# Kernel tuning notes

Hardware: AMD Instinct MI355X
Metric: run time of the kernel (lower is better)

The kernel has to match this reference:

```python
import jax, jax.numpy as jnp
import numpy as np

D = 256      # dim
H = 8        # num_heads
HD = D // H  # head dim
P = 256      # patch_size
B = 4        # num clouds
L = 32768    # points per cloud (divisible by P)
N = B * L
MLP = int(D * 2.0)
PEH = max(32, D // 4)
EPS = 1e-5


def setup_inputs() -> dict:
    key = jax.random.key(0)
    ks = jax.random.split(key, 20)
    s = 0.02
    w = lambda k, shp: jax.random.normal(k, shp, jnp.float32) * s
    inp = {
        "feats": jax.random.normal(ks[0], (N, D), jnp.float32),
        "coord": jax.random.uniform(ks[1], (N, 3), jnp.float32),
        "lengths": jnp.full((B,), L, jnp.int32),
        # CoordPositionalEncoding: Linear(3,PEH) -> ReLU -> Linear(PEH,D)
        "pe_w1": w(ks[2], (3, PEH)), "pe_b1": jnp.zeros((PEH,), jnp.float32),
        "pe_w2": w(ks[3], (PEH, D)), "pe_b2": jnp.zeros((D,), jnp.float32),
        "pre_g": jnp.ones((D,), jnp.float32), "pre_b": jnp.zeros((D,), jnp.float32),
        # block: norm1 + MHA + norm2 + MLP
        "n1_g": jnp.ones((D,), jnp.float32), "n1_b": jnp.zeros((D,), jnp.float32),
        "wqkv": w(ks[4], (D, 3 * D)), "bqkv": jnp.zeros((3 * D,), jnp.float32),
        "wo": w(ks[5], (D, D)), "bo": jnp.zeros((D,), jnp.float32),
        "n2_g": jnp.ones((D,), jnp.float32), "n2_b": jnp.zeros((D,), jnp.float32),
        "m_w1": w(ks[6], (D, MLP)), "m_b1": jnp.zeros((MLP,), jnp.float32),
        "m_w2": w(ks[7], (MLP, D)), "m_b2": jnp.zeros((D,), jnp.float32),
        # global_gate: Linear(2D,D)->ReLU->Linear(D,D)->Sigmoid
        "gg_w1": w(ks[8], (2 * D, D)), "gg_b1": jnp.zeros((D,), jnp.float32),
        "gg_w2": w(ks[9], (D, D)), "gg_b2": jnp.zeros((D,), jnp.float32),
        # fuse: Linear(2D,D)->ReLU->Linear(D,D)
        "f_w1": w(ks[10], (2 * D, D)), "f_b1": jnp.zeros((D,), jnp.float32),
        "f_w2": w(ks[11], (D, D)), "f_b2": jnp.zeros((D,), jnp.float32),
    }
    return inp


def _ln(x, g, b):
    m = x.mean(-1, keepdims=True)
    v = jnp.mean((x - m) ** 2, -1, keepdims=True)
    return (x - m) * jax.lax.rsqrt(v + EPS) * g + b


def _sgca(feats, coord, lengths,
          pe_w1, pe_b1, pe_w2, pe_b2, pre_g, pre_b,
          n1_g, n1_b, wqkv, bqkv, wo, bo, n2_g, n2_b,
          m_w1, m_b1, m_w2, m_b2,
          gg_w1, gg_b1, gg_w2, gg_b2, f_w1, f_b1, f_w2, f_b2):
    Bn = lengths.shape[0]
    Ln = feats.shape[0] // Bn  # equal-length clouds

    def cloud(f, c):  # f: [L, D], c: [L, 3]
        # positional encoding (per-cloud centered / max-abs scaled coords)
        cc = c - c.mean(0, keepdims=True)
        scale = jnp.clip(jnp.abs(cc).max(0, keepdims=True), 1e-6)
        pe = jax.nn.relu((cc / scale) @ pe_w1 + pe_b1) @ pe_w2 + pe_b2
        x = _ln(f + pe, pre_g, pre_b)
        # serialization order from min-max normalized coords
        cn = c - c.min(0, keepdims=True)
        cn = cn / jnp.clip(cn.max(0, keepdims=True), 1e-6)
        key = cn[:, 0] + 2.17 * cn[:, 1] + 3.31 * cn[:, 2]
        order = jnp.argsort(key)
        xs = x[order].reshape(-1, P, D)  # [NP, P, D] block-diagonal windows
        # attention block (pre-norm MHA + residual)
        h = _ln(xs, n1_g, n1_b)
        qkv = h @ wqkv + bqkv
        q = qkv[..., :D].reshape(-1, P, H, HD)
        k = qkv[..., D:2 * D].reshape(-1, P, H, HD)
        v = qkv[..., 2 * D:].reshape(-1, P, H, HD)
        scores = jnp.einsum('nphd,nqhd->nhpq', q, k) / np.sqrt(HD).astype(np.float32)
        a = jax.nn.softmax(scores, axis=-1)
        o = jnp.einsum('nhpq,nqhd->nphd', a, v).reshape(-1, P, D)
        xs = xs + (o @ wo + bo)
        # MLP + residual
        xs = xs + (jax.nn.gelu(_ln(xs, n2_g, n2_b) @ m_w1 + m_b1, approximate=False) @ m_w2 + m_b2)
        # undo serialization
        xo = xs.reshape(-1, D)[jnp.argsort(order)]
        # global token gate/fuse
        gt = jnp.broadcast_to(xo.mean(0, keepdims=True), xo.shape)
        gate = jax.nn.sigmoid(jax.nn.relu(jnp.concatenate([f, gt], -1) @ gg_w1 + gg_b1) @ gg_w2 + gg_b2)
        fused = jax.nn.relu(jnp.concatenate([xo, gt], -1) @ f_w1 + f_b1) @ f_w2 + f_b2
        return f + gate * fused

    out = jax.vmap(cloud)(feats.reshape(Bn, Ln, D), coord.reshape(Bn, Ln, 3))
    return out.reshape(-1, D)


def reference(feats, coord, lengths,
              pe_w1, pe_b1, pe_w2, pe_b2, pre_g, pre_b,
              n1_g, n1_b, wqkv, bqkv, wo, bo, n2_g, n2_b,
              m_w1, m_b1, m_w2, m_b2,
              gg_w1, gg_b1, gg_w2, gg_b2, f_w1, f_b1, f_w2, f_b2):
    return _sgca(feats, coord, lengths,
                 pe_w1, pe_b1, pe_w2, pe_b2, pre_g, pre_b,
                 n1_g, n1_b, wqkv, bqkv, wo, bo, n2_g, n2_b,
                 m_w1, m_b1, m_w2, m_b2,
                 gg_w1, gg_b1, gg_w2, gg_b2, f_w1, f_b1, f_w2, f_b2)
```

## Files before the change

kernel.cpp:

```cpp
#include <hip/hip_runtime.h>
#include <hip/hip_bf16.h>
#include <math.h>

#define D_DIM 256
#define NHEAD 8
#define HDIM 32
#define PATCH 256
#define NCLOUD 4
#define LPC 32768
#define NTOT (NCLOUD * LPC)
#define MLPD 512
#define PEHID 64
#define LN_EPS 1e-5f
#define NCHUNK 4
#define CROWS (NTOT / NCHUNK)

typedef unsigned long long u64;
typedef unsigned short u16;
typedef short bf16x8 __attribute__((ext_vector_type(8)));
typedef float f32x4 __attribute__((ext_vector_type(4)));

__device__ __forceinline__ u16 f2bf(float x) {
  unsigned u = __float_as_uint(x);
  u += 0x7fffu + ((u >> 16) & 1u);
  return (u16)(u >> 16);
}
__device__ __forceinline__ float bf2f(u16 u) {
  return __uint_as_float(((unsigned)u) << 16);
}

__device__ __forceinline__ void gload_lds16(const u16* g, u16* l) {
  __builtin_amdgcn_global_load_lds((const __attribute__((address_space(1))) void*)g,
                                   (__attribute__((address_space(3))) void*)l, 16, 0, 0);
}

__global__ __launch_bounds__(256) void stats_kernel(const float* __restrict__ coord,
                                                    float* __restrict__ stats) {
  const int c = blockIdx.x, t = threadIdx.x;
  float sm[3] = {0.f, 0.f, 0.f};
  float mn[3] = {1e30f, 1e30f, 1e30f};
  float mx[3] = {-1e30f, -1e30f, -1e30f};
  const float* cp = coord + (size_t)c * LPC * 3;
  for (int i = t; i < LPC; i += 256) {
#pragma unroll
    for (int a = 0; a < 3; a++) {
      float v = cp[(size_t)i * 3 + a];
      sm[a] += v;
      mn[a] = fminf(mn[a], v);
      mx[a] = fmaxf(mx[a], v);
    }
  }
  __shared__ float sb[256];
  float rsum[3], rmn[3], rmx[3];
#pragma unroll
  for (int a = 0; a < 3; a++) {
    sb[t] = sm[a]; __syncthreads();
    for (int s = 128; s > 0; s >>= 1) { if (t < s) sb[t] += sb[t + s]; __syncthreads(); }
    rsum[a] = sb[0]; __syncthreads();
    sb[t] = mn[a]; __syncthreads();
    for (int s = 128; s > 0; s >>= 1) { if (t < s) sb[t] = fminf(sb[t], sb[t + s]); __syncthreads(); }
    rmn[a] = sb[0]; __syncthreads();
    sb[t] = mx[a]; __syncthreads();
    for (int s = 128; s > 0; s >>= 1) { if (t < s) sb[t] = fmaxf(sb[t], sb[t + s]); __syncthreads(); }
    rmx[a] = sb[0]; __syncthreads();
  }
  if (t == 0) {
    float* st = stats + c * 16;
#pragma unroll
    for (int a = 0; a < 3; a++) {
      float mean = rsum[a] / (float)LPC;
      st[a] = mean;
      st[3 + a] = fmaxf(fmaxf(rmx[a] - mean, mean - rmn[a]), 1e-6f);
      st[6 + a] = rmn[a];
      st[9 + a] = fmaxf(rmx[a] - rmn[a], 1e-6f);
    }
  }
}

__global__ __launch_bounds__(256) void key_kernel(const float* __restrict__ coord,
                                                  const float* __restrict__ stats,
                                                  u64* __restrict__ keys) {
#pragma clang fp contract(off)
  const int g = blockIdx.x * 256 + threadIdx.x;
  const int c = g >> 15;
  const float* st = stats + c * 16;
  float k0 = (coord[(size_t)g * 3 + 0] - st[6]) / st[9];
  float k1 = (coord[(size_t)g * 3 + 1] - st[7]) / st[10];
  float k2 = (coord[(size_t)g * 3 + 2] - st[8]) / st[11];
  float key = k0 + 2.17f * k1;
  key = key + 3.31f * k2;
  keys[g] = ((u64)__float_as_uint(key) << 32) | (unsigned)(g & (LPC - 1));
}

__global__ __launch_bounds__(256) void sort_local_kernel(u64* __restrict__ keys) {
  __shared__ u64 s[4096];
  const int base = blockIdx.x * 4096;
  const int t = threadIdx.x;
  for (int i = t; i < 4096; i += 256) s[i] = keys[base + i];
  __syncthreads();
  for (int k = 2; k <= 4096; k <<= 1) {
    for (int j = k >> 1; j > 0; j >>= 1) {
      for (int p = t; p < 2048; p += 256) {
        int i = ((p & ~(j - 1)) << 1) | (p & (j - 1));
        int l = i | j;
        bool asc = (((base + i) & (LPC - 1)) & k) == 0;
        u64 a = s[i], bb = s[l];
        if (asc ? (a > bb) : (a < bb)) { s[i] = bb; s[l] = a; }
      }
      __syncthreads();
    }
  }
  for (int i = t; i < 4096; i += 256) keys[base + i] = s[i];
}

__global__ __launch_bounds__(256) void sort_global_kernel(u64* __restrict__ keys, int k, int j) {
  int p = blockIdx.x * 256 + threadIdx.x;
  int i = ((p & ~(j - 1)) << 1) | (p & (j - 1));
  int l = i | j;
  bool asc = ((i & (LPC - 1)) & k) == 0;
  u64 a = keys[i], b = keys[l];
  if (asc ? (a > b) : (a < b)) { keys[i] = b; keys[l] = a; }
}

__global__ __launch_bounds__(256) void sort_finish_kernel(u64* __restrict__ keys, int k) {
  __shared__ u64 s[4096];
  const int base = blockIdx.x * 4096;
  const int t = threadIdx.x;
  for (int i = t; i < 4096; i += 256) s[i] = keys[base + i];
  __syncthreads();
  for (int j = 2048; j > 0; j >>= 1) {
    for (int p = t; p < 2048; p += 256) {
      int i = ((p & ~(j - 1)) << 1) | (p & (j - 1));
      int l = i | j;
      bool asc = (((base + i) & (LPC - 1)) & k) == 0;
      u64 a = s[i], bb = s[l];
      if (asc ? (a > bb) : (a < bb)) { s[i] = bb; s[l] = a; }
    }
    __syncthreads();
  }
  for (int i = t; i < 4096; i += 256) keys[base + i] = s[i];
}

__global__ __launch_bounds__(256) void rank_kernel(const u64* __restrict__ keys,
                                                   int* __restrict__ order,
                                                   int* __restrict__ rank) {
  const int g = blockIdx.x * 256 + threadIdx.x;
  const int src = (int)(unsigned)(keys[g] & 0xffffffffULL) + (g & ~(LPC - 1));
  order[g] = src;
  rank[src] = g;
}

__global__ __launch_bounds__(256) void wtrans_kernel(const float* __restrict__ src,
                                                     u16* __restrict__ dst, int R, int C) {
  __shared__ float t[32][33];
  const int bx = blockIdx.x * 32, by = blockIdx.y * 32;
  const int lc = threadIdx.x & 31, lr = threadIdx.x >> 5;
  for (int i = 0; i < 32; i += 8) t[lr + i][lc] = src[(size_t)(by + lr + i) * C + bx + lc];
  __syncthreads();
  for (int i = 0; i < 32; i += 8)
    dst[(size_t)(bx + lr + i) * R + by + lc] = f2bf(t[lc][lr + i]);
}

__global__ __launch_bounds__(256) void conv_bf16_kernel(const float* __restrict__ in,
                                                        u16* __restrict__ out) {
  size_t i = ((size_t)blockIdx.x * 256 + threadIdx.x) * 4;
  float4 v = *(const float4*)(in + i);
  ushort4 o;
  o.x = f2bf(v.x); o.y = f2bf(v.y); o.z = f2bf(v.z); o.w = f2bf(v.w);
  *(ushort4*)(out + i) = o;
}

__global__ __launch_bounds__(256) void h_kernel(const float* __restrict__ coord,
                                                const float* __restrict__ stats,
                                                const float* __restrict__ pw1,
                                                const float* __restrict__ pb1,
                                                u16* __restrict__ H) {
  const int idx = blockIdx.x * 256 + threadIdx.x;
  const int row = idx >> 6, j = idx & 63;
  const int c = row >> 15;
  const float* st = stats + c * 16;
  float s0 = (coord[(size_t)row * 3 + 0] - st[0]) / st[3];
  float s1 = (coord[(size_t)row * 3 + 1] - st[1]) / st[4];
  float s2 = (coord[(size_t)row * 3 + 2] - st[2]) / st[5];
  float h = pb1[j] + s0 * pw1[j] + s1 * pw1[64 + j] + s2 * pw1[128 + j];
  H[idx] = f2bf(fmaxf(h, 0.f));
}

__global__ __launch_bounds__(256) void add_ln_kernel(const float* __restrict__ feats,
                                                     const u16* __restrict__ pe,
                                                     const int* __restrict__ rank,
                                                     const float* __restrict__ g,
                                                     const float* __restrict__ b,
                                                     float* __restrict__ xs) {
  const int row = blockIdx.x * 4 + (threadIdx.x >> 6);
  const int lane = threadIdx.x & 63;
  float4 f = *(const float4*)(feats + (size_t)row * 256 + lane * 4);
  ushort4 p = *(const ushort4*)(pe + (size_t)row * 256 + lane * 4);
  float v0 = f.x + bf2f(p.x), v1 = f.y + bf2f(p.y);
  float v2 = f.z + bf2f(p.z), v3 = f.w + bf2f(p.w);
  float s = v0 + v1 + v2 + v3;
#pragma unroll
  for (int o = 32; o > 0; o >>= 1) s += __shfl_xor(s, o);
  float mean = s * (1.f / 256.f);
  float d0 = v0 - mean, d1 = v1 - mean, d2 = v2 - mean, d3 = v3 - mean;
  float ss = d0 * d0 + d1 * d1 + d2 * d2 + d3 * d3;
#pragma unroll
  for (int o = 32; o > 0; o >>= 1) ss += __shfl_xor(ss, o);
  float inv = 1.f / sqrtf(ss * (1.f / 256.f) + LN_EPS);
  float4 gv = *(const float4*)(g + lane * 4);
  float4 bv = *(const float4*)(b + lane * 4);
  int dst = rank[row];
  float4 o4;
  o4.x = d0 * inv * gv.x + bv.x; o4.y = d1 * inv * gv.y + bv.y;
  o4.z = d2 * inv * gv.z + bv.z; o4.w = d3 * inv * gv.w + bv.w;
  *(float4*)(xs + (size_t)dst * 256 + lane * 4) = o4;
}

__global__ __launch_bounds__(256) void ln_bf16_kernel(const float* __restrict__ in,
                                                      const float* __restrict__ g,
                                                      const float* __restrict__ b,
                                                      u16* __restrict__ out) {
  const int row = blockIdx.x * 4 + (threadIdx.x >> 6);
  const int lane = threadIdx.x & 63;
  float4 v = *(const float4*)(in + (size_t)row * 256 + lane * 4);
  float s = v.x + v.y + v.z + v.w;
#pragma unroll
  for (int o = 32; o > 0; o >>= 1) s += __shfl_xor(s, o);
  float mean = s * (1.f / 256.f);
  float d0 = v.x - mean, d1 = v.y - mean, d2 = v.z - mean, d3 = v.w - mean;
  float ss = d0 * d0 + d1 * d1 + d2 * d2 + d3 * d3;
#pragma unroll
  for (int o = 32; o > 0; o >>= 1) ss += __shfl_xor(ss, o);
  float inv = 1.f / sqrtf(ss * (1.f / 256.f) + LN_EPS);
  float4 gv = *(const float4*)(g + lane * 4);
  float4 bv = *(const float4*)(b + lane * 4);
  ushort4 o4;
  o4.x = f2bf(d0 * inv * gv.x + bv.x); o4.y = f2bf(d1 * inv * gv.y + bv.y);
  o4.z = f2bf(d2 * inv * gv.z + bv.z); o4.w = f2bf(d3 * inv * gv.w + bv.w);
  *(ushort4*)(out + (size_t)row * 256 + lane * 4) = o4;
}

__global__ __launch_bounds__(256) void scatter_bf16_kernel(const int* __restrict__ order,
                                                           const float* __restrict__ xs,
                                                           u16* __restrict__ xo) {
  const int row = blockIdx.x * 4 + (threadIdx.x >> 6);
  const int lane = threadIdx.x & 63;
  float4 v = *(const float4*)(xs + (size_t)row * 256 + lane * 4);
  const int dst = order[row];
  ushort4 o;
  o.x = f2bf(v.x); o.y = f2bf(v.y); o.z = f2bf(v.z); o.w = f2bf(v.w);
  *(ushort4*)(xo + (size_t)dst * 256 + lane * 4) = o;
}

template <int K, int ACT, int MODE, bool EXTRA>
__global__ __launch_bounds__(256, 4) void mfma_gemm(const u16* __restrict__ A,
                                                    const u16* __restrict__ Wt,
                                                    const float* __restrict__ bias,
                                                    const float* __restrict__ extra,
                                                    void* __restrict__ Cout,
                                                    const u16* __restrict__ gate,
                                                    const float* __restrict__ feats, int Ko) {
  __shared__ __align__(16) u16 Al[128 * 32];
  __shared__ __align__(16) u16 Bl[128 * 32];
  const int tid = threadIdx.x;
  const int lane = tid & 63, wave = tid >> 6;
  const int wr = wave >> 1, wc = wave & 1;
  const int l15 = lane & 15, l4 = lane >> 4;
  const size_t row0 = (size_t)blockIdx.y * 128;
  const int col0 = blockIdx.x * 128;
  const int q0 = wave * 64 + lane;
  const int q1 = q0 + 256;
  const u16* gA0 = A + (row0 + (q0 >> 2)) * K + (q0 & 3) * 8;
  const u16* gA1 = A + (row0 + (q1 >> 2)) * K + (q1 & 3) * 8;
  const u16* gB0 = Wt + (size_t)(col0 + (q0 >> 2)) * K + (q0 & 3) * 8;
  const u16* gB1 = Wt + (size_t)(col0 + (q1 >> 2)) * K + (q1 & 3) * 8;
  u16* lA0 = Al + wave * 512;
  u16* lA1 = Al + 2048 + wave * 512;
  u16* lB0 = Bl + wave * 512;
  u16* lB1 = Bl + 2048 + wave * 512;
  f32x4 acc[4][4];
#pragma unroll
  for (int i = 0; i < 4; i++)
#pragma unroll
    for (int j = 0; j < 4; j++) acc[i][j] = f32x4{0.f, 0.f, 0.f, 0.f};
#pragma unroll 1
  for (int k0 = 0; k0 < K; k0 += 32) {
    gload_lds16(gA0 + k0, lA0);
    gload_lds16(gA1 + k0, lA1);
    gload_lds16(gB0 + k0, lB0);
    gload_lds16(gB1 + k0, lB1);
    __syncthreads();
    bf16x8 af[4], bfr[4];
#pragma unroll
    for (int rb = 0; rb < 4; rb++)
      af[rb] = *(const bf16x8*)&Al[(wr * 64 + rb * 16 + l15) * 32 + l4 * 8];
#pragma unroll
    for (int cb = 0; cb < 4; cb++)
      bfr[cb] = *(const bf16x8*)&Bl[(wc * 64 + cb * 16 + l15) * 32 + l4 * 8];
#pragma unroll
    for (int rb = 0; rb < 4; rb++)
#pragma unroll
      for (int cb = 0; cb < 4; cb++)
        acc[rb][cb] = __builtin_amdgcn_mfma_f32_16x16x32_bf16(af[rb], bfr[cb], acc[rb][cb], 0, 0, 0);
    __syncthreads();
  }
#pragma unroll
  for (int rb = 0; rb < 4; rb++)
#pragma unroll
    for (int cb = 0; cb < 4; cb++)
#pragma unroll
      for (int r = 0; r < 4; r++) {
        size_t row = row0 + wr * 64 + rb * 16 + l4 * 4 + r;
        int col = col0 + wc * 64 + cb * 16 + l15;
        float v = acc[rb][cb][r] + bias[col];
        if (EXTRA) v += extra[((int)(row >> 15)) * 256 + col];
        if (ACT == 1) v = fmaxf(v, 0.f);
        else if (ACT == 2) v = 0.5f * v * (1.f + erff(v * 0.70710678118654752440f));
        else if (ACT == 3) v = 1.f / (1.f + __expf(-v));
        size_t o = row * (size_t)Ko + col;
        if (MODE == 0) ((float*)Cout)[o] = v;
        else if (MODE == 1) ((float*)Cout)[o] += v;
        else if (MODE == 2) ((u16*)Cout)[o] = f2bf(v);
        else ((float*)Cout)[o] = feats[o] + bf2f(gate[o]) * v;
      }
}

__global__ __launch_bounds__(256, 3) void attn_mfma_kernel(const u16* __restrict__ qkv,
                                                           u16* __restrict__ ao) {
  __shared__ __align__(16) u16 VT[32 * 264];
  __shared__ __align__(16) u16 Pl[4][16 * 264];
  const int w = blockIdx.x, h = blockIdx.y;
  const int tid = threadIdx.x;
  const int lane = tid & 63, wave = tid >> 6;
  const int l15 = lane & 15, l4 = lane >> 4;
  const size_t base = (size_t)w * PATCH;
  {
    const u16* vrow = qkv + (base + tid) * 768 + 512 + h * HDIM;
#pragma unroll
    for (int d4 = 0; d4 < 8; d4++) {
      ushort4 v4 = *(const ushort4*)(vrow + d4 * 4);
      VT[(d4 * 4 + 0) * 264 + tid] = v4.x;
      VT[(d4 * 4 + 1) * 264 + tid] = v4.y;
      VT[(d4 * 4 + 2) * 264 + tid] = v4.z;
      VT[(d4 * 4 + 3) * 264 + tid] = v4.w;
    }
  }
  __syncthreads();
  u16* Pw = &Pl[wave][0];
  const float scale = 0.17677669529663687f;
  const f32x4 zero = {0.f, 0.f, 0.f, 0.f};
  for (int qt = 0; qt < 4; qt++) {
    const int qbase = wave * 64 + qt * 16;
    bf16x8 qf = *(const bf16x8*)(qkv + (base + qbase + l15) * 768 + h * HDIM + l4 * 8);
    f32x4 s[16];
#pragma unroll
    for (int kt = 0; kt < 16; kt++) {
      bf16x8 kf = *(const bf16x8*)(qkv + (base + kt * 16 + l15) * 768 + 256 + h * HDIM + l4 * 8);
      s[kt] = __builtin_amdgcn_mfma_f32_16x16x32_bf16(kf, qf, zero, 0, 0, 0);
    }
    float m = -1e30f;
#pragma unroll
    for (int kt = 0; kt < 16; kt++)
#pragma unroll
      for (int r = 0; r < 4; r++) { s[kt][r] *= scale; m = fmaxf(m, s[kt][r]); }
    m = fmaxf(m, __shfl_xor(m, 16));
    m = fmaxf(m, __shfl_xor(m, 32));
    float lsum = 0.f;
#pragma unroll
    for (int kt = 0; kt < 16; kt++) {
      float p0 = __expf(s[kt][0] - m), p1 = __expf(s[kt][1] - m);
      float p2 = __expf(s[kt][2] - m), p3 = __expf(s[kt][3] - m);
      lsum += (p0 + p1) + (p2 + p3);
      ushort4 pw4;
      pw4.x = f2bf(p0); pw4.y = f2bf(p1); pw4.z = f2bf(p2); pw4.w = f2bf(p3);
      *(ushort4*)&Pw[l15 * 264 + kt * 16 + l4 * 4] = pw4;
    }
    lsum += __shfl_xor(lsum, 16);
    lsum += __shfl_xor(lsum, 32);
    f32x4 o0 = zero, o1 = zero;
#pragma unroll
    for (int kc = 0; kc < 8; kc++) {
      bf16x8 pf = *(const bf16x8*)&Pw[l15 * 264 + kc * 32 + l4 * 8];
      bf16x8 va = *(const bf16x8*)&VT[l15 * 264 + kc * 32 + l4 * 8];
      bf16x8 vb = *(const bf16x8*)&VT[(16 + l15) * 264 + kc * 32 + l4 * 8];
      o0 = __builtin_amdgcn_mfma_f32_16x16x32_bf16(va, pf, o0, 0, 0, 0);
      o1 = __builtin_amdgcn_mfma_f32_16x16x32_bf16(vb, pf, o1, 0, 0, 0);
    }
    float inv = 1.f / lsum;
    u16* op = ao + (base + qbase + l15) * D_DIM + h * HDIM;
    ushort4 w0, w1;
    w0.x = f2bf(o0[0] * inv); w0.y = f2bf(o0[1] * inv);
    w0.z = f2bf(o0[2] * inv); w0.w = f2bf(o0[3] * inv);
    w1.x = f2bf(o1[0] * inv); w1.y = f2bf(o1[1] * inv);
    w1.z = f2bf(o1[2] * inv); w1.w = f2bf(o1[3] * inv);
    *(ushort4*)(op + l4 * 4) = w0;
    *(ushort4*)(op + 16 + l4 * 4) = w1;
  }
}

__global__ __launch_bounds__(256) void gt_partial_kernel(const float* __restrict__ xs,
                                                         float* __restrict__ part) {
  const int s = blockIdx.x, c = blockIdx.y;
  const int t = threadIdx.x;
  float acc = 0.f;
  const size_t base = (size_t)c * LPC + (size_t)s * 256;
  for (int r = 0; r < 256; r++) acc += xs[(base + r) * D_DIM + t];
  part[(size_t)(c * 128 + s) * D_DIM + t] = acc;
}

__global__ __launch_bounds__(256) void gt_reduce_kernel(const float* __restrict__ part,
                                                        float* __restrict__ gt) {
  const int c = blockIdx.x, t = threadIdx.x;
  float s = 0.f;
  for (int i = 0; i < 128; i++) s += part[(size_t)(c * 128 + i) * D_DIM + t];
  gt[c * D_DIM + t] = s * (1.f / (float)LPC);
}

__global__ __launch_bounds__(256) void pervec_kernel(const float* __restrict__ gt,
                                                     const float* __restrict__ ggw1,
                                                     const float* __restrict__ fw1,
                                                     float* __restrict__ ggt,
                                                     float* __restrict__ fgt) {
  const int c = blockIdx.x, which = blockIdx.y;
  const int t = threadIdx.x;
  const float* W = which ? fw1 : ggw1;
  float* o = which ? fgt : ggt;
  __shared__ float g[D_DIM];
  g[t] = gt[c * D_DIM + t];
  __syncthreads();
  float acc = 0.f;
#pragma unroll 8
  for (int k = 0; k < D_DIM; k++) acc += g[k] * W[(size_t)(256 + k) * D_DIM + t];
  o[c * D_DIM + t] = acc;
}

extern "C" void kernel_launch(void* const* d_in, const int* in_sizes, int n_in,
                              void* d_out, int out_size, void* d_ws, size_t ws_size,
                              hipStream_t stream) {
  const float* feats = (const float*)d_in[0];
  const float* coord = (const float*)d_in[1];
  const float* pe_w1 = (const float*)d_in[3];
  const float* pe_b1 = (const float*)d_in[4];
  const float* pe_w2 = (const float*)d_in[5];
  const float* pe_b2 = (const float*)d_in[6];
  const float* pre_g = (const float*)d_in[7];
  const float* pre_b = (const float*)d_in[8];
  const float* n1_g = (const float*)d_in[9];
  const float* n1_b = (const float*)d_in[10];
  const float* wqkv = (const float*)d_in[11];
  const float* bqkv = (const float*)d_in[12];
  const float* wo = (const float*)d_in[13];
  const float* bo = (const float*)d_in[14];
  const float* n2_g = (const float*)d_in[15];
  const float* n2_b = (const float*)d_in[16];
  const float* m_w1 = (const float*)d_in[17];
  const float* m_b1 = (const float*)d_in[18];
  const float* m_w2 = (const float*)d_in[19];
  const float* m_b2 = (const float*)d_in[20];
  const float* gg_w1 = (const float*)d_in[21];
  const float* gg_b1 = (const float*)d_in[22];
  const float* gg_w2 = (const float*)d_in[23];
  const float* gg_b2 = (const float*)d_in[24];
  const float* f_w1 = (const float*)d_in[25];
  const float* f_b1 = (const float*)d_in[26];
  const float* f_w2 = (const float*)d_in[27];
  const float* f_b2 = (const float*)d_in[28];
  float* out = (float*)d_out;

  char* ws = (char*)d_ws;
  float* xs = (float*)(ws);
  u16* hbuf = (u16*)(ws + 134217728);
  u16* qkvchunk = (u16*)(ws + 201326592);
  u16* aochunk = (u16*)(ws + 251658240);
  u16* tbuf = (u16*)(ws + 268435456);
  u16* Hbuf = (u16*)(ws + 268435456);
  u16* xobf = (u16*)(ws + 201326592);
  size_t off = 301989888;
  u64* keybuf = (u64*)(ws + off); off += (size_t)NTOT * 8;
  int* orderbuf = (int*)(ws + off); off += (size_t)NTOT * 4;
  int* rankbuf = (int*)(ws + off); off += (size_t)NTOT * 4;
  float* statsbuf = (float*)(ws + off); off += 4096;
  float* gtpart = (float*)(ws + off); off += (size_t)NCLOUD * 128 * D_DIM * 4;
  float* gtbuf = (float*)(ws + off); off += 4096;
  float* ggtbuf = (float*)(ws + off); off += 4096;
  float* fgtbuf = (float*)(ws + off); off += 4096;
  u16* wqkvT = (u16*)(ws + off); off += 768 * 256 * 2;
  u16* woT = (u16*)(ws + off); off += 256 * 256 * 2;
  u16* mw1T = (u16*)(ws + off); off += 512 * 256 * 2;
  u16* mw2T = (u16*)(ws + off); off += 256 * 512 * 2;
  u16* ggw1T = (u16*)(ws + off); off += 256 * 256 * 2;
  u16* ggw2T = (u16*)(ws + off); off += 256 * 256 * 2;
  u16* fw1T = (u16*)(ws + off); off += 256 * 256 * 2;
  u16* fw2T = (u16*)(ws + off); off += 256 * 256 * 2;
  u16* pw2T = (u16*)(ws + off); off += 64 * 256 * 2;
  u16* featsbf = (u16*)(ws);
  u16* gatebuf = (u16*)(ws + 67108864);

  stats_kernel<<<NCLOUD, 256, 0, stream>>>(coord, statsbuf);
  key_kernel<<<NTOT / 256, 256, 0, stream>>>(coord, statsbuf, keybuf);
  sort_local_kernel<<<NTOT / 4096, 256, 0, stream>>>(keybuf);
  for (int k = 8192; k <= 32768; k <<= 1) {
    for (int j = k >> 1; j >= 4096; j >>= 1)
      sort_global_kernel<<<NTOT / 512, 256, 0, stream>>>(keybuf, k, j);
    sort_finish_kernel<<<NTOT / 4096, 256, 0, stream>>>(keybuf, k);
  }
  rank_kernel<<<NTOT / 256, 256, 0, stream>>>(keybuf, orderbuf, rankbuf);
  wtrans_kernel<<<dim3(24, 8), 256, 0, stream>>>(wqkv, wqkvT, 256, 768);
  wtrans_kernel<<<dim3(8, 8), 256, 0, stream>>>(wo, woT, 256, 256);
  wtrans_kernel<<<dim3(16, 8), 256, 0, stream>>>(m_w1, mw1T, 256, 512);
  wtrans_kernel<<<dim3(8, 16), 256, 0, stream>>>(m_w2, mw2T, 512, 256);
  wtrans_kernel<<<dim3(8, 8), 256, 0, stream>>>(gg_w1, ggw1T, 256, 256);
  wtrans_kernel<<<dim3(8, 8), 256, 0, stream>>>(gg_w2, ggw2T, 256, 256);
  wtrans_kernel<<<dim3(8, 8), 256, 0, stream>>>(f_w1, fw1T, 256, 256);
  wtrans_kernel<<<dim3(8, 8), 256, 0, stream>>>(f_w2, fw2T, 256, 256);
  wtrans_kernel<<<dim3(8, 2), 256, 0, stream>>>(pe_w2, pw2T, 64, 256);
  h_kernel<<<NTOT * 64 / 256, 256, 0, stream>>>(coord, statsbuf, pe_w1, pe_b1, Hbuf);
  mfma_gemm<64, 0, 2, false><<<dim3(2, NTOT / 128), 256, 0, stream>>>(
      Hbuf, pw2T, pe_b2, nullptr, hbuf, nullptr, nullptr, 256);
  add_ln_kernel<<<NTOT / 4, 256, 0, stream>>>(feats, hbuf, rankbuf, pre_g, pre_b, xs);
  ln_bf16_kernel<<<NTOT / 4, 256, 0, stream>>>(xs, n1_g, n1_b, hbuf);
  for (int ch = 0; ch < NCHUNK; ch++) {
    const size_t ro = (size_t)ch * CROWS;
    mfma_gemm<256, 0, 2, false><<<dim3(6, CROWS / 128), 256, 0, stream>>>(
        hbuf + ro * 256, wqkvT, bqkv, nullptr, qkvchunk, nullptr, nullptr, 768);
    attn_mfma_kernel<<<dim3(CROWS / PATCH, NHEAD), 256, 0, stream>>>(qkvchunk, aochunk);
    mfma_gemm<256, 0, 1, false><<<dim3(2, CROWS / 128), 256, 0, stream>>>(
        aochunk, woT, bo, nullptr, xs + ro * 256, nullptr, nullptr, 256);
  }
  ln_bf16_kernel<<<NTOT / 4, 256, 0, stream>>>(xs, n2_g, n2_b, hbuf);
  for (int ch = 0; ch < NCHUNK; ch++) {
    const size_t ro = (size_t)ch * CROWS;
    mfma_gemm<256, 2, 2, false><<<dim3(MLPD / 128, CROWS / 128), 256, 0, stream>>>(
        hbuf + ro * 256, mw1T, m_b1, nullptr, tbuf, nullptr, nullptr, 512);
    mfma_gemm<512, 0, 1, false><<<dim3(2, CROWS / 128), 256, 0, stream>>>(
        tbuf, mw2T, m_b2, nullptr, xs + ro * 256, nullptr, nullptr, 256);
  }
  scatter_bf16_kernel<<<NTOT / 4, 256, 0, stream>>>(orderbuf, xs, xobf);
  gt_partial_kernel<<<dim3(128, NCLOUD), 256, 0, stream>>>(xs, gtpart);
  gt_reduce_kernel<<<NCLOUD, 256, 0, stream>>>(gtpart, gtbuf);
  pervec_kernel<<<dim3(NCLOUD, 2), 256, 0, stream>>>(gtbuf, gg_w1, f_w1, ggtbuf, fgtbuf);
  conv_bf16_kernel<<<NTOT * 256 / 1024, 256, 0, stream>>>(feats, featsbf);
  mfma_gemm<256, 1, 2, true><<<dim3(2, NTOT / 128), 256, 0, stream>>>(
      featsbf, ggw1T, gg_b1, ggtbuf, hbuf, nullptr, nullptr, 256);
  mfma_gemm<256, 3, 2, false><<<dim3(2, NTOT / 128), 256, 0, stream>>>(
      hbuf, ggw2T, gg_b2, nullptr, gatebuf, nullptr, nullptr, 256);
  mfma_gemm<256, 1, 2, true><<<dim3(2, NTOT / 128), 256, 0, stream>>>(
      xobf, fw1T, f_b1, fgtbuf, hbuf, nullptr, nullptr, 256);
  mfma_gemm<256, 0, 3, false><<<dim3(2, NTOT / 128), 256, 0, stream>>>(
      hbuf, fw2T, f_b2, nullptr, out, gatebuf, feats, 256);
  (void)in_sizes; (void)n_in; (void)out_size; (void)ws_size;
}
```

Baseline: 1.539 ms.

## Fuse gate and fuse second-layer GEMMs into one kernel; widen sort blocks

Replaces the separate sigmoid-gate GEMM and the final fuse GEMM with a single dual-GEMM kernel that computes both products per tile and applies feats + sigmoid(g)*f directly. This removes the bf16 gate buffer round trip and one kernel launch. The catch is doubled LDS and accumulator registers, with occupancy lowered to 2 blocks per SM. Separately, the bitonic local and finish sort kernels now run with 1024 threads per block instead of 256, so each thread does fewer compare-exchange iterations per stage.

```diff
diff --git a/kernel.cpp b/kernel.cpp
--- a/kernel.cpp
+++ b/kernel.cpp
@@ -92,15 +92,15 @@
   keys[g] = ((u64)__float_as_uint(key) << 32) | (unsigned)(g & (LPC - 1));
 }
 
-__global__ __launch_bounds__(256) void sort_local_kernel(u64* __restrict__ keys) {
+__global__ __launch_bounds__(1024) void sort_local_kernel(u64* __restrict__ keys) {
   __shared__ u64 s[4096];
   const int base = blockIdx.x * 4096;
   const int t = threadIdx.x;
-  for (int i = t; i < 4096; i += 256) s[i] = keys[base + i];
+  for (int i = t; i < 4096; i += 1024) s[i] = keys[base + i];
   __syncthreads();
   for (int k = 2; k <= 4096; k <<= 1) {
     for (int j = k >> 1; j > 0; j >>= 1) {
-      for (int p = t; p < 2048; p += 256) {
+      for (int p = t; p < 2048; p += 1024) {
         int i = ((p & ~(j - 1)) << 1) | (p & (j - 1));
         int l = i | j;
         bool asc = (((base + i) & (LPC - 1)) & k) == 0;
@@ -110,7 +110,7 @@
       __syncthreads();
     }
   }
-  for (int i = t; i < 4096; i += 256) keys[base + i] = s[i];
+  for (int i = t; i < 4096; i += 1024) keys[base + i] = s[i];
 }
 
 __global__ __launch_bounds__(256) void sort_global_kernel(u64* __restrict__ keys, int k, int j) {
@@ -122,14 +122,14 @@
   if (asc ? (a > b) : (a < b)) { keys[i] = b; keys[l] = a; }
 }
 
-__global__ __launch_bounds__(256) void sort_finish_kernel(u64* __restrict__ keys, int k) {
+__global__ __launch_bounds__(1024) void sort_finish_kernel(u64* __restrict__ keys, int k) {
   __shared__ u64 s[4096];
   const int base = blockIdx.x * 4096;
   const int t = threadIdx.x;
-  for (int i = t; i < 4096; i += 256) s[i] = keys[base + i];
+  for (int i = t; i < 4096; i += 1024) s[i] = keys[base + i];
   __syncthreads();
   for (int j = 2048; j > 0; j >>= 1) {
-    for (int p = t; p < 2048; p += 256) {
+    for (int p = t; p < 2048; p += 1024) {
       int i = ((p & ~(j - 1)) << 1) | (p & (j - 1));
       int l = i | j;
       bool asc = (((base + i) & (LPC - 1)) & k) == 0;
@@ -138,7 +138,7 @@
     }
     __syncthreads();
   }
-  for (int i = t; i < 4096; i += 256) keys[base + i] = s[i];
+  for (int i = t; i < 4096; i += 1024) keys[base + i] = s[i];
 }
 
 __global__ __launch_bounds__(256) void rank_kernel(const u64* __restrict__ keys,
@@ -257,9 +257,7 @@
                                                     const u16* __restrict__ Wt,
                                                     const float* __restrict__ bias,
                                                     const float* __restrict__ extra,
-                                                    void* __restrict__ Cout,
-                                                    const u16* __restrict__ gate,
-                                                    const float* __restrict__ feats, int Ko) {
+                                                    void* __restrict__ Cout, int Ko) {
   __shared__ __align__(16) u16 Al[128 * 32];
   __shared__ __align__(16) u16 Bl[128 * 32];
   const int tid = threadIdx.x;
@@ -320,8 +318,79 @@
         size_t o = row * (size_t)Ko + col;
         if (MODE == 0) ((float*)Cout)[o] = v;
         else if (MODE == 1) ((float*)Cout)[o] += v;
-        else if (MODE == 2) ((u16*)Cout)[o] = f2bf(v);
-        else ((float*)Cout)[o] = feats[o] + bf2f(gate[o]) * v;
+        else ((u16*)Cout)[o] = f2bf(v);
+      }
+}
+
+__global__ __launch_bounds__(256, 2) void fuse2_kernel(const u16* __restrict__ A1,
+                                                       const u16* __restrict__ A2,
+                                                       const u16* __restrict__ B1t,
+                                                       const u16* __restrict__ B2t,
+                                                       const float* __restrict__ bias1,
+                                                       const float* __restrict__ bias2,
+                                                       const float* __restrict__ feats,
+                                                       float* __restrict__ out) {
+  __shared__ __align__(16) u16 A1l[128 * 32];
+  __shared__ __align__(16) u16 A2l[128 * 32];
+  __shared__ __align__(16) u16 B1l[128 * 32];
+  __shared__ __align__(16) u16 B2l[128 * 32];
+  const int tid = threadIdx.x;
+  const int lane = tid & 63, wave = tid >> 6;
+  const int wr = wave >> 1, wc = wave & 1;
+  const int l15 = lane & 15, l4 = lane >> 4;
+  const size_t row0 = (size_t)blockIdx.y * 128;
+  const int col0 = blockIdx.x * 128;
+  const int q0 = wave * 64 + lane;
+  const int q1 = q0 + 256;
+  const size_t a0off = (row0 + (q0 >> 2)) * 256 + (q0 & 3) * 8;
+  const size_t a1off = (row0 + (q1 >> 2)) * 256 + (q1 & 3) * 8;
+  const size_t b0off = (size_t)(col0 + (q0 >> 2)) * 256 + (q0 & 3) * 8;
+  const size_t b1off = (size_t)(col0 + (q1 >> 2)) * 256 + (q1 & 3) * 8;
+  f32x4 acc1[4][4], acc2[4][4];
+#pragma unroll
+  for (int i = 0; i < 4; i++)
+#pragma unroll
+    for (int j = 0; j < 4; j++) {
+      acc1[i][j] = f32x4{0.f, 0.f, 0.f, 0.f};
+      acc2[i][j] = f32x4{0.f, 0.f, 0.f, 0.f};
+    }
+#pragma unroll 1
+  for (int k0 = 0; k0 < 256; k0 += 32) {
+    gload_lds16(A1 + a0off + k0, A1l + wave * 512);
+    gload_lds16(A1 + a1off + k0, A1l + 2048 + wave * 512);
+    gload_lds16(A2 + a0off + k0, A2l + wave * 512);
+    gload_lds16(A2 + a1off + k0, A2l + 2048 + wave * 512);
+    gload_lds16(B1t + b0off + k0, B1l + wave * 512);
+    gload_lds16(B1t + b1off + k0, B1l + 2048 + wave * 512);
+    gload_lds16(B2t + b0off + k0, B2l + wave * 512);
+    gload_lds16(B2t + b1off + k0, B2l + 2048 + wave * 512);
+    __syncthreads();
+#pragma unroll
+    for (int rb = 0; rb < 4; rb++) {
+      bf16x8 a1f = *(const bf16x8*)&A1l[(wr * 64 + rb * 16 + l15) * 32 + l4 * 8];
+      bf16x8 a2f = *(const bf16x8*)&A2l[(wr * 64 + rb * 16 + l15) * 32 + l4 * 8];
+#pragma unroll
+      for (int cb = 0; cb < 4; cb++) {
+        bf16x8 b1f = *(const bf16x8*)&B1l[(wc * 64 + cb * 16 + l15) * 32 + l4 * 8];
+        bf16x8 b2f = *(const bf16x8*)&B2l[(wc * 64 + cb * 16 + l15) * 32 + l4 * 8];
+        acc1[rb][cb] = __builtin_amdgcn_mfma_f32_16x16x32_bf16(a1f, b1f, acc1[rb][cb], 0, 0, 0);
+        acc2[rb][cb] = __builtin_amdgcn_mfma_f32_16x16x32_bf16(a2f, b2f, acc2[rb][cb], 0, 0, 0);
+      }
+    }
+    __syncthreads();
+  }
+#pragma unroll
+  for (int rb = 0; rb < 4; rb++)
+#pragma unroll
+    for (int cb = 0; cb < 4; cb++)
+#pragma unroll
+      for (int r = 0; r < 4; r++) {
+        size_t row = row0 + wr * 64 + rb * 16 + l4 * 4 + r;
+        int col = col0 + wc * 64 + cb * 16 + l15;
+        float g = 1.f / (1.f + __expf(-(acc1[rb][cb][r] + bias1[col])));
+        float fv = acc2[rb][cb][r] + bias2[col];
+        size_t o = row * 256 + col;
+        out[o] = feats[o] + g * fv;
       }
 }
 
@@ -494,15 +563,15 @@
   u16* fw2T = (u16*)(ws + off); off += 256 * 256 * 2;
   u16* pw2T = (u16*)(ws + off); off += 64 * 256 * 2;
   u16* featsbf = (u16*)(ws);
-  u16* gatebuf = (u16*)(ws + 67108864);
+  u16* u1buf = (u16*)(ws + 67108864);
 
   stats_kernel<<<NCLOUD, 256, 0, stream>>>(coord, statsbuf);
   key_kernel<<<NTOT / 256, 256, 0, stream>>>(coord, statsbuf, keybuf);
-  sort_local_kernel<<<NTOT / 4096, 256, 0, stream>>>(keybuf);
+  sort_local_kernel<<<NTOT / 4096, 1024, 0, stream>>>(keybuf);
   for (int k = 8192; k <= 32768; k <<= 1) {
     for (int j = k >> 1; j >= 4096; j >>= 1)
       sort_global_kernel<<<NTOT / 512, 256, 0, stream>>>(keybuf, k, j);
-    sort_finish_kernel<<<NTOT / 4096, 256, 0, stream>>>(keybuf, k);
+    sort_finish_kernel<<<NTOT / 4096, 1024, 0, stream>>>(keybuf, k);
   }
   rank_kernel<<<NTOT / 256, 256, 0, stream>>>(keybuf, orderbuf, rankbuf);
   wtrans_kernel<<<dim3(24, 8), 256, 0, stream>>>(wqkv, wqkvT, 256, 768);
@@ -516,24 +585,24 @@
   wtrans_kernel<<<dim3(8, 2), 256, 0, stream>>>(pe_w2, pw2T, 64, 256);
   h_kernel<<<NTOT * 64 / 256, 256, 0, stream>>>(coord, statsbuf, pe_w1, pe_b1, Hbuf);
   mfma_gemm<64, 0, 2, false><<<dim3(2, NTOT / 128), 256, 0, stream>>>(
-      Hbuf, pw2T, pe_b2, nullptr, hbuf, nullptr, nullptr, 256);
+      Hbuf, pw2T, pe_b2, nullptr, hbuf, 256);
   add_ln_kernel<<<NTOT / 4, 256, 0, stream>>>(feats, hbuf, rankbuf, pre_g, pre_b, xs);
   ln_bf16_kernel<<<NTOT / 4, 256, 0, stream>>>(xs, n1_g, n1_b, hbuf);
   for (int ch = 0; ch < NCHUNK; ch++) {
     const size_t ro = (size_t)ch * CROWS;
     mfma_gemm<256, 0, 2, false><<<dim3(6, CROWS / 128), 256, 0, stream>>>(
-        hbuf + ro * 256, wqkvT, bqkv, nullptr, qkvchunk, nullptr, nullptr, 768);
+        hbuf + ro * 256, wqkvT, bqkv, nullptr, qkvchunk, 768);
     attn_mfma_kernel<<<dim3(CROWS / PATCH, NHEAD), 256, 0, stream>>>(qkvchunk, aochunk);
     mfma_gemm<256, 0, 1, false><<<dim3(2, CROWS / 128), 256, 0, stream>>>(
-        aochunk, woT, bo, nullptr, xs + ro * 256, nullptr, nullptr, 256);
+        aochunk, woT, bo, nullptr, xs + ro * 256, 256);
   }
   ln_bf16_kernel<<<NTOT / 4, 256, 0, stream>>>(xs, n2_g, n2_b, hbuf);
   for (int ch = 0; ch < NCHUNK; ch++) {
     const size_t ro = (size_t)ch * CROWS;
     mfma_gemm<256, 2, 2, false><<<dim3(MLPD / 128, CROWS / 128), 256, 0, stream>>>(
-        hbuf + ro * 256, mw1T, m_b1, nullptr, tbuf, nullptr, nullptr, 512);
+        hbuf + ro * 256, mw1T, m_b1, nullptr, tbuf, 512);
     mfma_gemm<512, 0, 1, false><<<dim3(2, CROWS / 128), 256, 0, stream>>>(
-        tbuf, mw2T, m_b2, nullptr, xs + ro * 256, nullptr, nullptr, 256);
+        tbuf, mw2T, m_b2, nullptr, xs + ro * 256, 256);
   }
   scatter_bf16_kernel<<<NTOT / 4, 256, 0, stream>>>(orderbuf, xs, xobf);
   gt_partial_kernel<<<dim3(128, NCLOUD), 256, 0, stream>>>(xs, gtpart);
@@ -541,12 +610,10 @@
   pervec_kernel<<<dim3(NCLOUD, 2), 256, 0, stream>>>(gtbuf, gg_w1, f_w1, ggtbuf, fgtbuf);
   conv_bf16_kernel<<<NTOT * 256 / 1024, 256, 0, stream>>>(feats, featsbf);
   mfma_gemm<256, 1, 2, true><<<dim3(2, NTOT / 128), 256, 0, stream>>>(
-      featsbf, ggw1T, gg_b1, ggtbuf, hbuf, nullptr, nullptr, 256);
-  mfma_gemm<256, 3, 2, false><<<dim3(2, NTOT / 128), 256, 0, stream>>>(
-      hbuf, ggw2T, gg_b2, nullptr, gatebuf, nullptr, nullptr, 256);
+      featsbf, ggw1T, gg_b1, ggtbuf, hbuf, 256);
   mfma_gemm<256, 1, 2, true><<<dim3(2, NTOT / 128), 256, 0, stream>>>(
-      xobf, fw1T, f_b1, fgtbuf, hbuf, nullptr, nullptr, 256);
-  mfma_gemm<256, 0, 3, false><<<dim3(2, NTOT / 128), 256, 0, stream>>>(
-      hbuf, fw2T, f_b2, nullptr, out, gatebuf, feats, 256);
+      xobf, fw1T, f_b1, fgtbuf, u1buf, 256);
+  fuse2_kernel<<<dim3(2, NTOT / 128), 256, 0, stream>>>(
+      hbuf, u1buf, ggw2T, fw2T, gg_b2, f_b2, feats, out);
   (void)in_sizes; (void)n_in; (void)out_size; (void)ws_size;
 }
```

Result: faster. 1.422 ms (-7.6%).
